# Performance work log

Measured on AMD Instinct MI355X. Metric: run time of the kernel, lower is better.

The kernel has to match this reference:

```python
import jax, jax.numpy as jnp
import numpy as np

N_WITHIN = 20   # n_labels for active dataset (cityscapes)
N_CROSS = 27    # n_labels for other dataset (idd)
ALPHA = 0.5
BETA = 0.5
T = 1.0


def _l2norm_rows(w):
    return w / jnp.sqrt(jnp.sum(w * w, axis=1, keepdims=True) + 1e-12)


def setup_inputs() -> dict:
    key = jax.random.key(0)
    k1, k2, k3, k4 = jax.random.split(key, 4)
    B, D, H, W = 4, 64, 512, 512
    encoder_op = jax.random.normal(k1, (B, D, H, W), jnp.float32)
    # conv weights are row-normalized label embeddings (frozen in original)
    w_within = _l2norm_rows(jax.random.normal(k2, (N_WITHIN, D), jnp.float32))
    w_cross = _l2norm_rows(jax.random.normal(k3, (N_CROSS, D), jnp.float32))
    targets = jax.random.randint(k4, (B, H, W), 0, N_WITHIN, dtype=jnp.int32)
    return {"encoder_op": encoder_op, "w_within": w_within,
            "w_cross": w_cross, "targets": targets}


def _entropy_loss(logits):
    # mean over (b,h,w) of -sum_c p * log p, softmax over channel dim 1
    logp = jax.nn.log_softmax(logits, axis=1)
    p = jnp.exp(logp)
    return jnp.mean(-jnp.sum(p * logp, axis=1)).reshape(-1)


def reference(encoder_op, w_within, w_cross, targets):
    # 1x1 conv == channel contraction; drop last (background) channel as in torch code
    within_map = jnp.einsum('bdhw,nd->bnhw', encoder_op, w_within)[:, :-1]
    cross_map = jnp.einsum('bdhw,nd->bnhw', encoder_op, w_cross)[:, :-1] / T
    loss_unsup = ALPHA * _entropy_loss(cross_map) + BETA * _entropy_loss(within_map)

    # _update_centroids: per-label masked sum == segment_sum over flattened pixels
    B, D, H, W = encoder_op.shape
    feats = encoder_op.transpose(0, 2, 3, 1).reshape(-1, D)  # [B*H*W, D]
    labs = targets.reshape(-1)                               # [B*H*W]
    centroids = jax.ops.segment_sum(feats, labs, num_segments=N_WITHIN)  # [N, D]
    counts = jax.ops.segment_sum(jnp.ones_like(labs, dtype=jnp.int32), labs,
                                 num_segments=N_WITHIN)                   # [N]
    # original detaches centroids (.data)
    return loss_unsup, jax.lax.stop_gradient(centroids), counts
```

## Files before the change

### kernel.cpp

```cpp
#include <hip/hip_runtime.h>
#include <hip/hip_bf16.h>

#define HW_   (512 * 512)
#define B_    4
#define D_    64
#define NPIX  (B_ * HW_)
#define NW    19
#define NC    26
#define NSEG  20
#define SW_   20
#define SC_   28
#define THREADS 256

#define L19(X) X(0)X(1)X(2)X(3)X(4)X(5)X(6)X(7)X(8)X(9)X(10)X(11)X(12)X(13)X(14)X(15)X(16)X(17)X(18)
#define L26(X) X(0)X(1)X(2)X(3)X(4)X(5)X(6)X(7)X(8)X(9)X(10)X(11)X(12)X(13)X(14)X(15)X(16)X(17)X(18)X(19)X(20)X(21)X(22)X(23)X(24)X(25)

__global__ void transpose_w(const float* __restrict__ wW, const float* __restrict__ wC,
                            float* __restrict__ ws) {
    int i = blockIdx.x * 256 + threadIdx.x;
    float* wTW = ws;
    float* wTC = ws + D_ * SW_;
    if (i < D_ * SW_) {
        int c = i / SW_, n = i - c * SW_;
        wTW[i] = (n < NW) ? wW[n * D_ + c] : 0.f;
    }
    if (i < D_ * SC_) {
        int c = i / SC_, n = i - c * SC_;
        wTC[i] = (n < NC) ? wC[n * D_ + c] : 0.f;
    }
}

__global__ __launch_bounds__(THREADS)
void fused_embed(const float* __restrict__ enc, const float* __restrict__ ws,
                 const int* __restrict__ targ, float* __restrict__ out)
{
    const float* wTW = ws;
    const float* wTC = ws + D_ * SW_;

    __shared__ float sCent[NSEG][D_ + 1];
    __shared__ int   sCount[NSEG];
    __shared__ float sRed[THREADS / 64];

    const int tid = threadIdx.x;
    for (int i = tid; i < NSEG * (D_ + 1); i += THREADS) (&sCent[0][0])[i] = 0.f;
    if (tid < NSEG) sCount[tid] = 0;
    __syncthreads();

    const int p   = blockIdx.x * THREADS + tid;
    const int b   = (blockIdx.x * THREADS) / HW_;
    const int hw0 = p - b * HW_;
    const float* fp = enc + (size_t)b * (D_ * HW_) + hw0;
    const int lab = targ[p];

#pragma unroll
    for (int c0 = 0; c0 < D_; c0 += 8) {
        float g0 = fp[(size_t)(c0 + 0) * HW_];
        float g1 = fp[(size_t)(c0 + 1) * HW_];
        float g2 = fp[(size_t)(c0 + 2) * HW_];
        float g3 = fp[(size_t)(c0 + 3) * HW_];
        float g4 = fp[(size_t)(c0 + 4) * HW_];
        float g5 = fp[(size_t)(c0 + 5) * HW_];
        float g6 = fp[(size_t)(c0 + 6) * HW_];
        float g7 = fp[(size_t)(c0 + 7) * HW_];
        atomicAdd(&sCent[lab][c0 + 0], g0);
        atomicAdd(&sCent[lab][c0 + 1], g1);
        atomicAdd(&sCent[lab][c0 + 2], g2);
        atomicAdd(&sCent[lab][c0 + 3], g3);
        atomicAdd(&sCent[lab][c0 + 4], g4);
        atomicAdd(&sCent[lab][c0 + 5], g5);
        atomicAdd(&sCent[lab][c0 + 6], g6);
        atomicAdd(&sCent[lab][c0 + 7], g7);
    }
    atomicAdd(&sCount[lab], 1);

    float lossAcc = 0.f;

    {
#define DECL(n) float a##n = 0.f;
        L19(DECL)
#undef DECL
#pragma unroll 1
        for (int c = 0; c < D_; c += 2) {
            float f0 = fp[(size_t)c * HW_];
            float f1 = fp[(size_t)(c + 1) * HW_];
            const float* r0 = wTW + c * SW_;
            const float* r1 = r0 + SW_;
#define FMA2(n) { a##n = fmaf(r0[n], f0, a##n); a##n = fmaf(r1[n], f1, a##n); }
            L19(FMA2)
#undef FMA2
        }
        float S = 0.f, Wt = 0.f;
#define ES(n) { float e = __expf(a##n); S += e; Wt = fmaf(e, a##n, Wt); }
        L19(ES)
#undef ES
        lossAcc += __logf(S) - Wt / S;
    }

    {
#define DECL(n) float a##n = 0.f;
        L26(DECL)
#undef DECL
#pragma unroll 1
        for (int c = 0; c < D_; c += 2) {
            float f0 = fp[(size_t)c * HW_];
            float f1 = fp[(size_t)(c + 1) * HW_];
            const float* r0 = wTC + c * SC_;
            const float* r1 = r0 + SC_;
#define FMA2(n) { a##n = fmaf(r0[n], f0, a##n); a##n = fmaf(r1[n], f1, a##n); }
            L26(FMA2)
#undef FMA2
        }
        float S = 0.f, Wt = 0.f;
#define ES(n) { float e = __expf(a##n); S += e; Wt = fmaf(e, a##n, Wt); }
        L26(ES)
#undef ES
        lossAcc += __logf(S) - Wt / S;
    }

#pragma unroll
    for (int off = 32; off; off >>= 1) lossAcc += __shfl_down(lossAcc, off);
    if ((tid & 63) == 0) sRed[tid >> 6] = lossAcc;
    __syncthreads();
    if (tid == 0) {
        float s = 0.f;
#pragma unroll
        for (int w = 0; w < THREADS / 64; ++w) s += sRed[w];
        atomicAdd(out, s * (0.5f / (float)NPIX));
    }

    for (int i = tid; i < NSEG * D_; i += THREADS) {
        int n = i >> 6, d = i & 63;
        atomicAdd(&out[1 + i], sCent[n][d]);
    }
    if (tid < NSEG) atomicAdd(&out[1 + NSEG * D_ + tid], (float)sCount[tid]);
}

extern "C" void kernel_launch(void* const* d_in, const int* in_sizes, int n_in,
                              void* d_out, int out_size, void* d_ws, size_t ws_size,
                              hipStream_t stream) {
    const float* enc = (const float*)d_in[0];
    const float* wW  = (const float*)d_in[1];
    const float* wC  = (const float*)d_in[2];
    const int*   targ = (const int*)d_in[3];
    float* out = (float*)d_out;
    float* ws  = (float*)d_ws;

    hipMemsetAsync(d_out, 0, (size_t)out_size * sizeof(float), stream);

    transpose_w<<<dim3((D_ * SC_ + 255) / 256), dim3(256), 0, stream>>>(wW, wC, ws);
    fused_embed<<<dim3(NPIX / THREADS), dim3(THREADS), 0, stream>>>(enc, ws, targ, out);
}
```

Before: 380.9 us.

## Process four pixel chunks per block and replace global atomics with partial-sum reduction

Each block now processes four 256-pixel chunks, so the grid shrinks from 4096 to 1024 blocks and per-block shared-memory init and flush costs are spread over more pixels. Instead of atomically adding 1281 centroid and count values per block into the output, each block writes its partials to a workspace slice, and a separate reduce kernel sums them. This also removes the memset. The risk is less parallelism per launch, which may hide memory latency less well, plus an extra kernel launch and the workspace traffic it needs.

```diff
diff --git a/kernel.cpp b/kernel.cpp
--- a/kernel.cpp
+++ b/kernel.cpp
@@ -1,5 +1,4 @@
 #include <hip/hip_runtime.h>
-#include <hip/hip_bf16.h>
 
 #define HW_   (512 * 512)
 #define B_    4
@@ -10,7 +9,12 @@
 #define NSEG  20
 #define SW_   20
 #define SC_   28
+#define WFLOATS (D_ * SW_ + D_ * SC_)
 #define THREADS 256
+#define NBLK  1024
+#define CHUNKS 4
+#define PSTRIDE 1312
+#define NOUT  1301
 
 #define L19(X) X(0)X(1)X(2)X(3)X(4)X(5)X(6)X(7)X(8)X(9)X(10)X(11)X(12)X(13)X(14)X(15)X(16)X(17)X(18)
 #define L26(X) X(0)X(1)X(2)X(3)X(4)X(5)X(6)X(7)X(8)X(9)X(10)X(11)X(12)X(13)X(14)X(15)X(16)X(17)X(18)X(19)X(20)X(21)X(22)X(23)X(24)X(25)
@@ -32,7 +36,7 @@
 
 __global__ __launch_bounds__(THREADS)
 void fused_embed(const float* __restrict__ enc, const float* __restrict__ ws,
-                 const int* __restrict__ targ, float* __restrict__ out)
+                 const int* __restrict__ targ, float* __restrict__ part)
 {
     const float* wTW = ws;
     const float* wTC = ws + D_ * SW_;
@@ -46,93 +50,104 @@
     if (tid < NSEG) sCount[tid] = 0;
     __syncthreads();
 
-    const int p   = blockIdx.x * THREADS + tid;
-    const int b   = (blockIdx.x * THREADS) / HW_;
-    const int hw0 = p - b * HW_;
-    const float* fp = enc + (size_t)b * (D_ * HW_) + hw0;
-    const int lab = targ[p];
-
-#pragma unroll
-    for (int c0 = 0; c0 < D_; c0 += 8) {
-        float g0 = fp[(size_t)(c0 + 0) * HW_];
-        float g1 = fp[(size_t)(c0 + 1) * HW_];
-        float g2 = fp[(size_t)(c0 + 2) * HW_];
-        float g3 = fp[(size_t)(c0 + 3) * HW_];
-        float g4 = fp[(size_t)(c0 + 4) * HW_];
-        float g5 = fp[(size_t)(c0 + 5) * HW_];
-        float g6 = fp[(size_t)(c0 + 6) * HW_];
-        float g7 = fp[(size_t)(c0 + 7) * HW_];
-        atomicAdd(&sCent[lab][c0 + 0], g0);
-        atomicAdd(&sCent[lab][c0 + 1], g1);
-        atomicAdd(&sCent[lab][c0 + 2], g2);
-        atomicAdd(&sCent[lab][c0 + 3], g3);
-        atomicAdd(&sCent[lab][c0 + 4], g4);
-        atomicAdd(&sCent[lab][c0 + 5], g5);
-        atomicAdd(&sCent[lab][c0 + 6], g6);
-        atomicAdd(&sCent[lab][c0 + 7], g7);
-    }
-    atomicAdd(&sCount[lab], 1);
+    const int blk0 = blockIdx.x * (THREADS * CHUNKS);
+    const int b    = blk0 / HW_;
+    const float* base = enc + (size_t)b * (D_ * HW_) - (size_t)b * HW_;
 
     float lossAcc = 0.f;
 
-    {
+#pragma unroll 1
+    for (int k = 0; k < CHUNKS; ++k) {
+        const int p = blk0 + k * THREADS + tid;
+        const float* fp = base + p;
+        const int lab = targ[p];
+
+#pragma unroll
+        for (int c0 = 0; c0 < D_; c0 += 8) {
+            float g0 = fp[(size_t)(c0 + 0) * HW_];
+            float g1 = fp[(size_t)(c0 + 1) * HW_];
+            float g2 = fp[(size_t)(c0 + 2) * HW_];
+            float g3 = fp[(size_t)(c0 + 3) * HW_];
+            float g4 = fp[(size_t)(c0 + 4) * HW_];
+            float g5 = fp[(size_t)(c0 + 5) * HW_];
+            float g6 = fp[(size_t)(c0 + 6) * HW_];
+            float g7 = fp[(size_t)(c0 + 7) * HW_];
+            atomicAdd(&sCent[lab][c0 + 0], g0);
+            atomicAdd(&sCent[lab][c0 + 1], g1);
+            atomicAdd(&sCent[lab][c0 + 2], g2);
+            atomicAdd(&sCent[lab][c0 + 3], g3);
+            atomicAdd(&sCent[lab][c0 + 4], g4);
+            atomicAdd(&sCent[lab][c0 + 5], g5);
+            atomicAdd(&sCent[lab][c0 + 6], g6);
+            atomicAdd(&sCent[lab][c0 + 7], g7);
+        }
+        atomicAdd(&sCount[lab], 1);
+
+        {
 #define DECL(n) float a##n = 0.f;
-        L19(DECL)
+            L19(DECL)
 #undef DECL
 #pragma unroll 1
-        for (int c = 0; c < D_; c += 2) {
-            float f0 = fp[(size_t)c * HW_];
-            float f1 = fp[(size_t)(c + 1) * HW_];
-            const float* r0 = wTW + c * SW_;
-            const float* r1 = r0 + SW_;
+            for (int c = 0; c < D_; c += 2) {
+                float f0 = fp[(size_t)c * HW_];
+                float f1 = fp[(size_t)(c + 1) * HW_];
+                const float* r0 = wTW + c * SW_;
+                const float* r1 = r0 + SW_;
 #define FMA2(n) { a##n = fmaf(r0[n], f0, a##n); a##n = fmaf(r1[n], f1, a##n); }
-            L19(FMA2)
+                L19(FMA2)
 #undef FMA2
+            }
+            float S = 0.f, Wt = 0.f;
+#define ES(n) { float e = __expf(a##n); S += e; Wt = fmaf(e, a##n, Wt); }
+            L19(ES)
+#undef ES
+            lossAcc += __logf(S) - Wt / S;
         }
-        float S = 0.f, Wt = 0.f;
-#define ES(n) { float e = __expf(a##n); S += e; Wt = fmaf(e, a##n, Wt); }
-        L19(ES)
-#undef ES
-        lossAcc += __logf(S) - Wt / S;
-    }
 
-    {
+        {
 #define DECL(n) float a##n = 0.f;
-        L26(DECL)
+            L26(DECL)
 #undef DECL
 #pragma unroll 1
-        for (int c = 0; c < D_; c += 2) {
-            float f0 = fp[(size_t)c * HW_];
-            float f1 = fp[(size_t)(c + 1) * HW_];
-            const float* r0 = wTC + c * SC_;
-            const float* r1 = r0 + SC_;
+            for (int c = 0; c < D_; c += 2) {
+                float f0 = fp[(size_t)c * HW_];
+                float f1 = fp[(size_t)(c + 1) * HW_];
+                const float* r0 = wTC + c * SC_;
+                const float* r1 = r0 + SC_;
 #define FMA2(n) { a##n = fmaf(r0[n], f0, a##n); a##n = fmaf(r1[n], f1, a##n); }
-            L26(FMA2)
+                L26(FMA2)
 #undef FMA2
+            }
+            float S = 0.f, Wt = 0.f;
+#define ES(n) { float e = __expf(a##n); S += e; Wt = fmaf(e, a##n, Wt); }
+            L26(ES)
+#undef ES
+            lossAcc += __logf(S) - Wt / S;
         }
-        float S = 0.f, Wt = 0.f;
-#define ES(n) { float e = __expf(a##n); S += e; Wt = fmaf(e, a##n, Wt); }
-        L26(ES)
-#undef ES
-        lossAcc += __logf(S) - Wt / S;
     }
 
 #pragma unroll
     for (int off = 32; off; off >>= 1) lossAcc += __shfl_down(lossAcc, off);
     if ((tid & 63) == 0) sRed[tid >> 6] = lossAcc;
     __syncthreads();
-    if (tid == 0) {
-        float s = 0.f;
-#pragma unroll
-        for (int w = 0; w < THREADS / 64; ++w) s += sRed[w];
-        atomicAdd(out, s * (0.5f / (float)NPIX));
-    }
 
+    float* my = part + (size_t)blockIdx.x * PSTRIDE;
+    if (tid == 0) my[0] = sRed[0] + sRed[1] + sRed[2] + sRed[3];
     for (int i = tid; i < NSEG * D_; i += THREADS) {
         int n = i >> 6, d = i & 63;
-        atomicAdd(&out[1 + i], sCent[n][d]);
+        my[1 + i] = sCent[n][d];
     }
-    if (tid < NSEG) atomicAdd(&out[1 + NSEG * D_ + tid], (float)sCount[tid]);
+    if (tid < NSEG) my[1 + NSEG * D_ + tid] = (float)sCount[tid];
+}
+
+__global__ void reduce_part(const float* __restrict__ part, float* __restrict__ out) {
+    int o = blockIdx.x * 256 + threadIdx.x;
+    if (o >= NOUT) return;
+    float s = 0.f;
+    const float* p = part + o;
+#pragma unroll 8
+    for (int b = 0; b < NBLK; ++b) s += p[(size_t)b * PSTRIDE];
+    out[o] = (o == 0) ? s * (0.5f / (float)NPIX) : s;
 }
 
 extern "C" void kernel_launch(void* const* d_in, const int* in_sizes, int n_in,
@@ -144,9 +159,9 @@
     const int*   targ = (const int*)d_in[3];
     float* out = (float*)d_out;
     float* ws  = (float*)d_ws;
-
-    hipMemsetAsync(d_out, 0, (size_t)out_size * sizeof(float), stream);
+    float* part = ws + WFLOATS;
 
     transpose_w<<<dim3((D_ * SC_ + 255) / 256), dim3(256), 0, stream>>>(wW, wC, ws);
-    fused_embed<<<dim3(NPIX / THREADS), dim3(THREADS), 0, stream>>>(enc, ws, targ, out);
+    fused_embed<<<dim3(NBLK), dim3(THREADS), 0, stream>>>(enc, ws, targ, part);
+    reduce_part<<<dim3((NOUT + 255) / 256), dim3(256), 0, stream>>>(part, out);
 }
```

Measured after the change: 453.2 us. 1.19x slower.
